# Performance work log

Hardware: AMD Instinct MI355X
Metric: run time of the kernel (lower is better)

The kernel has to match this reference:

```python
import jax, jax.numpy as jnp
import numpy as np

DIM = 1024
NUM_HEADS = 16
HEAD_DIM = DIM // NUM_HEADS
SCALE = HEAD_DIM ** -0.5
NEG = -1e9


def setup_inputs() -> dict:
    key = jax.random.key(0)
    ks = jax.random.split(key, 10)
    B, N, M, C = 8, 1024, 1024, DIM
    q = jax.random.normal(ks[0], (B, N, C), jnp.float32)
    k = jax.random.normal(ks[1], (B, M, C), jnp.float32)
    v = jax.random.normal(ks[2], (B, M, C), jnp.float32)
    mask = jax.random.randint(ks[3], (B, N), 0, 2, jnp.int32)
    target_mask = jax.random.randint(ks[4], (B, N, M), 0, 2, jnp.int32)
    Wq = jax.random.normal(ks[5], (C, C), jnp.float32) * 0.02
    Wk = jax.random.normal(ks[6], (C, C), jnp.float32) * 0.02
    Wv = jax.random.normal(ks[7], (C, C), jnp.float32) * 0.02
    Wo = jax.random.normal(ks[8], (C, C), jnp.float32) * 0.02
    bo = jnp.zeros((C,), jnp.float32)
    return {"q": q, "k": k, "v": v, "mask": mask, "target_mask": target_mask,
            "Wq": Wq, "Wk": Wk, "Wv": Wv, "Wo": Wo, "bo": bo}


def reference(q, k, v, mask, target_mask, Wq, Wk, Wv, Wo, bo):
    B, N, C = q.shape
    M = k.shape[1]
    H, D = NUM_HEADS, HEAD_DIM
    qh = (q @ Wq).reshape(B, N, H, D)
    kh = (k @ Wk).reshape(B, M, H, D)
    vh = (v @ Wv).reshape(B, M, H, D)
    attn = jnp.einsum('bnhd,bmhd->bhnm', qh, kh) * SCALE  # (B,H,N,M)
    # self-attn key mask (B,N) -> broadcast over queries (requires N==M as in original)
    attn = jnp.where(mask[:, None, None, :] == 0, NEG, attn)
    # cross-attn mask (B,N,M) -> broadcast over heads
    attn = jnp.where(target_mask[:, None, :, :] == 0, NEG, attn)
    attn = jax.nn.softmax(attn, axis=-1)
    x = jnp.einsum('bhnm,bmhd->bnhd', attn, vh).reshape(B, N, C)
    return x @ Wo + bo
```

## Files before the change

kernel.cpp:

```cpp
#include <hip/hip_runtime.h>
#include <hip/hip_bf16.h>

#define DEV __device__ __forceinline__

typedef __attribute__((ext_vector_type(8))) short bf16x8;
typedef __attribute__((ext_vector_type(4))) float f32x4;
typedef unsigned int u32;
typedef unsigned long long u64;

#define VMCNT(n) asm volatile("s_waitcnt vmcnt(" #n ")" ::: "memory")

DEV short f2bf(float f) {
  union { float f; u32 u; } x; x.f = f;
  u32 r = x.u + 0x7fffu + ((x.u >> 16) & 1u);
  return (short)(r >> 16);
}

DEV void gload_lds16(const void* g, void* l) {
  __builtin_amdgcn_global_load_lds(
      (const __attribute__((address_space(1))) u32*)g,
      (__attribute__((address_space(3))) u32*)l, 16, 0, 0);
}

DEV bf16x8 frag(const short* L, int row, int col) {
  return *(const bf16x8*)&L[row * 64 + (col ^ ((row & 7) << 3))];
}

DEV void stageA256(const char* base, int ktb, char* lds, int w, int lane) {
  int r8 = lane >> 3;
  int csw = ((lane & 7) ^ r8) << 4;
#pragma unroll
  for (int l = 0; l < 4; ++l) {
    int c = l * 8 + w;
    gload_lds16(base + (size_t)(c * 8 + r8) * 2048 + ktb + csw, lds + c * 1024);
  }
}
DEV void stageB128(const char* base, int ktb, char* lds, int w, int lane) {
  int r8 = lane >> 3;
  int csw = ((lane & 7) ^ r8) << 4;
#pragma unroll
  for (int l = 0; l < 2; ++l) {
    int c = l * 8 + w;
    gload_lds16(base + (size_t)(c * 8 + r8) * 2048 + ktb + csw, lds + c * 1024);
  }
}

DEV void tile_compute(const short* Asb, const short* Bsb, f32x4 acc[8][2],
                      int wm, int wn, int lr, int lg) {
  bf16x8 bfrag[2][2];
#pragma unroll
  for (int ni = 0; ni < 2; ++ni)
#pragma unroll
    for (int ks = 0; ks < 2; ++ks)
      bfrag[ni][ks] = frag(Bsb, wn * 32 + ni * 16 + lr, ks * 32 + lg * 8);
#pragma unroll
  for (int pi = 0; pi < 4; ++pi) {
    bf16x8 af[2][2];
#pragma unroll
    for (int m2 = 0; m2 < 2; ++m2)
#pragma unroll
      for (int ks = 0; ks < 2; ++ks)
        af[m2][ks] = frag(Asb, wm * 128 + (pi * 2 + m2) * 16 + lr, ks * 32 + lg * 8);
    __builtin_amdgcn_s_setprio(1);
#pragma unroll
    for (int m2 = 0; m2 < 2; ++m2)
#pragma unroll
      for (int ni = 0; ni < 2; ++ni)
#pragma unroll
        for (int ks = 0; ks < 2; ++ks)
          acc[pi * 2 + m2][ni] = __builtin_amdgcn_mfma_f32_16x16x32_bf16(
              af[m2][ks], bfrag[ni][ks], acc[pi * 2 + m2][ni], 0, 0, 0);
    __builtin_amdgcn_s_setprio(0);
  }
}

#define ENTRY_SYNC()                          \
  __builtin_amdgcn_sched_barrier(0);          \
  __builtin_amdgcn_s_barrier();               \
  __builtin_amdgcn_sched_barrier(0)

__global__ __launch_bounds__(256) void prologue(
    const float* __restrict__ q, const float* __restrict__ k, const float* __restrict__ v,
    short* __restrict__ qb, short* __restrict__ kb, short* __restrict__ vb,
    const float* __restrict__ W0, const float* __restrict__ W1,
    const float* __restrict__ W2, const float* __restrict__ W3,
    short* __restrict__ WtAll,
    const int* __restrict__ mask, const int* __restrict__ tmask, u64* __restrict__ pk) {
  int bx = blockIdx.x;
  if (bx < 12288) {
    int z = bx >> 12, bi = bx & 4095;
    const float* src = z == 0 ? q : z == 1 ? k : v;
    short* dst = z == 0 ? qb : z == 1 ? kb : vb;
    size_t i = ((size_t)bi * 256 + threadIdx.x) * 8;
    float4 f0 = *(const float4*)(src + i);
    float4 f1 = *(const float4*)(src + i + 4);
    bf16x8 o;
    o[0] = f2bf(f0.x); o[1] = f2bf(f0.y); o[2] = f2bf(f0.z); o[3] = f2bf(f0.w);
    o[4] = f2bf(f1.x); o[5] = f2bf(f1.y); o[6] = f2bf(f1.z); o[7] = f2bf(f1.w);
    *(bf16x8*)(dst + i) = o;
  } else if (bx < 13312) {
    int idx = bx - 12288;
    int z = idx >> 8, rem = idx & 255;
    const float* W = z == 0 ? W0 : z == 1 ? W1 : z == 2 ? W2 : W3;
    short* Wt = WtAll + (size_t)z * 1024 * 1024;
    __shared__ short tile[64][65];
    int k0 = (rem >> 4) * 64, n0 = (rem & 15) * 64;
    int t = threadIdx.x;
    int r = t >> 2, c = (t & 3) * 16;
    const float* src = W + (size_t)(k0 + r) * 1024 + n0 + c;
#pragma unroll
    for (int i = 0; i < 16; i += 4) {
      float4 f = *(const float4*)(src + i);
      tile[r][c + i + 0] = f2bf(f.x);
      tile[r][c + i + 1] = f2bf(f.y);
      tile[r][c + i + 2] = f2bf(f.z);
      tile[r][c + i + 3] = f2bf(f.w);
    }
    __syncthreads();
    bf16x8 v0, v1;
#pragma unroll
    for (int i = 0; i < 8; ++i) v0[i] = tile[c + i][r];
#pragma unroll
    for (int i = 0; i < 8; ++i) v1[i] = tile[c + 8 + i][r];
    short* dst = Wt + (size_t)(n0 + r) * 1024 + k0 + c;
    *(bf16x8*)(dst) = v0;
    *(bf16x8*)(dst + 8) = v1;
  } else {
    int bn = bx - 13312;
    int b = bn >> 10;
    int t = threadIdx.x, w = t >> 6, lane = t & 63;
    const int* tr = tmask + (size_t)bn * 1024;
    const int* mr = mask + b * 1024;
#pragma unroll
    for (int it = 0; it < 4; ++it) {
      int m = it * 256 + w * 64 + lane;
      bool on = (mr[m] != 0) && (tr[m] != 0);
      u64 bits = __ballot(on);
      if (lane == 0) pk[(size_t)bn * 16 + it * 4 + w] = bits;
    }
  }
}

__global__ __launch_bounds__(256) void vtrans(const short* __restrict__ vh,
                                              short* __restrict__ vht) {
  __shared__ short tile[64][65];
  int m0 = blockIdx.x * 64;
  int bh = blockIdx.y;
  int t = threadIdx.x;
  int r = t >> 2, c = (t & 3) * 16;
  const short* src = vh + ((size_t)bh * 1024 + m0 + r) * 64 + c;
  bf16x8 a0 = *(const bf16x8*)(src);
  bf16x8 a1 = *(const bf16x8*)(src + 8);
#pragma unroll
  for (int i = 0; i < 8; ++i) tile[r][c + i] = a0[i];
#pragma unroll
  for (int i = 0; i < 8; ++i) tile[r][c + 8 + i] = a1[i];
  __syncthreads();
  bf16x8 v0, v1;
#pragma unroll
  for (int i = 0; i < 8; ++i) v0[i] = tile[c + i][r];
#pragma unroll
  for (int i = 0; i < 8; ++i) v1[i] = tile[c + 8 + i][r];
  short* dst = vht + ((size_t)bh * 64 + r) * 1024 + m0 + c;
  *(bf16x8*)dst = v0;
  *(bf16x8*)(dst + 8) = v1;
}

#define QSCALE 0.18033688011112042f

__global__ __launch_bounds__(512, 2) void gemm_qkv(
    const short* __restrict__ qb, const short* __restrict__ kb, const short* __restrict__ vb,
    const short* __restrict__ WtAll,
    short* __restrict__ qh, short* __restrict__ kh, short* __restrict__ vh) {
  __shared__ __align__(16) short AsAll[3 * 256 * 64];
  __shared__ __align__(16) short BsAll[3 * 128 * 64];

  int flat = blockIdx.y * 8 + blockIdx.x;
  int nid = (flat & 7) * 96 + (flat >> 3);
  int zz = nid >> 8;
  int rr = nid & 255;
  int bm = (rr >> 3) * 256, bn = (rr & 7) * 128;

  const short* A; short* Ch; float cs;
  if (zz == 0)      { A = qb; Ch = qh; cs = QSCALE; }
  else if (zz == 1) { A = kb; Ch = kh; cs = 1.0f; }
  else              { A = vb; Ch = vh; cs = 1.0f; }
  const short* Wt = WtAll + (size_t)zz * 1024 * 1024;

  int tid = threadIdx.x;
  int lane = tid & 63, w = tid >> 6;
  int wm = w >> 2, wn = w & 3;
  int lr = lane & 15, lg = lane >> 4;

  const f32x4 fz = {0.f, 0.f, 0.f, 0.f};
  f32x4 acc[8][2];
#pragma unroll
  for (int i = 0; i < 8; ++i) { acc[i][0] = fz; acc[i][1] = fz; }

  const char* abase = (const char*)A + (size_t)bm * 2048;
  const char* bbase = (const char*)Wt + (size_t)bn * 2048;

  stageA256(abase, 0, (char*)AsAll, w, lane);
  stageB128(bbase, 0, (char*)BsAll, w, lane);
  stageA256(abase, 128, (char*)AsAll + 32768, w, lane);
  stageB128(bbase, 128, (char*)BsAll + 16384, w, lane);

  int cb = 0, sb = 2;
  for (int t = 0; t < 15; ++t) {
    VMCNT(6);
    ENTRY_SYNC();
    if (t < 14) {
      stageA256(abase, (t + 2) * 128, (char*)AsAll + sb * 32768, w, lane);
      stageB128(bbase, (t + 2) * 128, (char*)BsAll + sb * 16384, w, lane);
    }
    tile_compute(AsAll + cb * 16384, BsAll + cb * 8192, acc, wm, wn, lr, lg);
    cb = (cb == 2) ? 0 : cb + 1;
    sb = (sb == 2) ? 0 : sb + 1;
  }
  VMCNT(0);
  ENTRY_SYNC();
  tile_compute(AsAll + cb * 16384, BsAll + cb * 8192, acc, wm, wn, lr, lg);

#pragma unroll
  for (int mi = 0; mi < 8; ++mi)
#pragma unroll
    for (int ni = 0; ni < 2; ++ni) {
      int ccol = bn + wn * 32 + ni * 16 + lr;
      int h = ccol >> 6, d = ccol & 63;
#pragma unroll
      for (int j = 0; j < 4; ++j) {
        int r = bm + wm * 128 + mi * 16 + lg * 4 + j;
        int bb = r >> 10, n = r & 1023;
        Ch[(((size_t)bb * 16 + h) * 1024 + n) * 64 + d] = f2bf(acc[mi][ni][j] * cs);
      }
    }
}

__global__ __launch_bounds__(512, 2) void gemm_out(
    const short* __restrict__ X, const short* __restrict__ Wot,
    const float* __restrict__ bo, float* __restrict__ out) {
  __shared__ __align__(16) short AsAll[3 * 256 * 64];
  __shared__ __align__(16) short BsAll[3 * 128 * 64];

  int flat = blockIdx.y * 8 + blockIdx.x;
  int nid = (flat & 7) * 32 + (flat >> 3);
  int bm = (nid >> 3) * 256, bn = (nid & 7) * 128;

  int tid = threadIdx.x;
  int lane = tid & 63, w = tid >> 6;
  int wm = w >> 2, wn = w & 3;
  int lr = lane & 15, lg = lane >> 4;

  const f32x4 fz = {0.f, 0.f, 0.f, 0.f};
  f32x4 acc[8][2];
#pragma unroll
  for (int i = 0; i < 8; ++i) { acc[i][0] = fz; acc[i][1] = fz; }

  const char* abase = (const char*)X + (size_t)bm * 2048;
  const char* bbase = (const char*)Wot + (size_t)bn * 2048;

  stageA256(abase, 0, (char*)AsAll, w, lane);
  stageB128(bbase, 0, (char*)BsAll, w, lane);
  stageA256(abase, 128, (char*)AsAll + 32768, w, lane);
  stageB128(bbase, 128, (char*)BsAll + 16384, w, lane);

  int cb = 0, sb = 2;
  for (int t = 0; t < 15; ++t) {
    VMCNT(6);
    ENTRY_SYNC();
    if (t < 14) {
      stageA256(abase, (t + 2) * 128, (char*)AsAll + sb * 32768, w, lane);
      stageB128(bbase, (t + 2) * 128, (char*)BsAll + sb * 16384, w, lane);
    }
    tile_compute(AsAll + cb * 16384, BsAll + cb * 8192, acc, wm, wn, lr, lg);
    cb = (cb == 2) ? 0 : cb + 1;
    sb = (sb == 2) ? 0 : sb + 1;
  }
  VMCNT(0);
  ENTRY_SYNC();
  tile_compute(AsAll + cb * 16384, BsAll + cb * 8192, acc, wm, wn, lr, lg);

#pragma unroll
  for (int mi = 0; mi < 8; ++mi)
#pragma unroll
    for (int ni = 0; ni < 2; ++ni) {
      int ccol = bn + wn * 32 + ni * 16 + lr;
      float bias = bo[ccol];
#pragma unroll
      for (int j = 0; j < 4; ++j) {
        int r = bm + wm * 128 + mi * 16 + lg * 4 + j;
        out[(size_t)r * 1024 + ccol] = acc[mi][ni][j] + bias;
      }
    }
}

DEV void stage_kv(const char* kbase, const char* vbase, int kv0,
                  short* Ksb, short* Vsb, int w, int lane) {
#pragma unroll
  for (int i = 0; i < 2; ++i) {
    int c = w * 2 + i;
    int row = (lane >> 3);
    int colb = ((lane & 7) ^ row) << 4;
    gload_lds16(kbase + (size_t)(kv0 + c * 8 + row) * 128 + colb, (char*)Ksb + c * 1024);
    gload_lds16(vbase + (size_t)(c * 8 + row) * 2048 + kv0 * 2 + colb, (char*)Vsb + c * 1024);
  }
}

__global__ __launch_bounds__(256, 2) void attn(
    const short* __restrict__ qh, const short* __restrict__ kh, const short* __restrict__ vht,
    const u64* __restrict__ pk, short* __restrict__ x) {
  __shared__ __align__(16) short Ks[2][4096];
  __shared__ __align__(16) short Vs[2][4096];
  __shared__ __align__(16) short Ps[2][8192];

  int flat = blockIdx.y * 8 + blockIdx.x;
  int nid = (flat & 7) * 64 + (flat >> 3);
  int bh = nid >> 2, qp = nid & 3;
  int b = bh >> 4;
  int tid = threadIdx.x, lane = tid & 63, w = tid >> 6;
  int lr = lane & 15, lg = lane >> 4;

  bf16x8 qa[2][2][2];
#pragma unroll
  for (int sub = 0; sub < 2; ++sub) {
    const short* qb2 = qh + ((size_t)bh * 1024 + qp * 256 + sub * 128 + w * 32) * 64;
#pragma unroll
    for (int mi = 0; mi < 2; ++mi)
#pragma unroll
      for (int ks = 0; ks < 2; ++ks)
        qa[sub][mi][ks] = *(const bf16x8*)(qb2 + (mi * 16 + lr) * 64 + ks * 32 + lg * 8);
  }

  const f32x4 fz = {0.f, 0.f, 0.f, 0.f};
  f32x4 o[2][2][4];
  float psum[2][2][4];
#pragma unroll
  for (int sub = 0; sub < 2; ++sub)
#pragma unroll
    for (int mi = 0; mi < 2; ++mi)
#pragma unroll
      for (int j = 0; j < 4; ++j) { psum[sub][mi][j] = 0.f; o[sub][mi][j] = fz; }

  const char* kbase = (const char*)(kh + (size_t)bh * 65536);
  const char* vbase = (const char*)(vht + (size_t)bh * 65536);
  const u64* pkb = pk + ((size_t)b * 1024 + qp * 256) * 16;

  stage_kv(kbase, vbase, 0, Ks[0], Vs[0], w, lane);
  __syncthreads();
  int cur = 0;

  for (int t = 0; t < 16; ++t) {
    if (t < 15) stage_kv(kbase, vbase, (t + 1) * 64, Ks[cur ^ 1], Vs[cur ^ 1], w, lane);

#pragma unroll
    for (int sub = 0; sub < 2; ++sub) {
      u64 pw[2][4];
#pragma unroll
      for (int mi = 0; mi < 2; ++mi)
#pragma unroll
        for (int j = 0; j < 4; ++j)
          pw[mi][j] = pkb[(sub * 128 + w * 32 + mi * 16 + lg * 4 + j) * 16 + t];

      f32x4 s[2][4];
#pragma unroll
      for (int mi = 0; mi < 2; ++mi)
#pragma unroll
        for (int ni = 0; ni < 4; ++ni) s[mi][ni] = fz;
      __builtin_amdgcn_s_setprio(1);
#pragma unroll
      for (int ks = 0; ks < 2; ++ks) {
        bf16x8 kb2[4];
#pragma unroll
        for (int ni = 0; ni < 4; ++ni)
          kb2[ni] = *(const bf16x8*)&Ks[cur][(ni * 16 + lr) * 64 + ((ks * 32 + lg * 8) ^ ((lr & 7) << 3))];
#pragma unroll
        for (int mi = 0; mi < 2; ++mi)
#pragma unroll
          for (int ni = 0; ni < 4; ++ni)
            s[mi][ni] = __builtin_amdgcn_mfma_f32_16x16x32_bf16(qa[sub][mi][ks], kb2[ni], s[mi][ni], 0, 0, 0);
      }
      __builtin_amdgcn_s_setprio(0);

#pragma unroll
      for (int mi = 0; mi < 2; ++mi)
#pragma unroll
        for (int j = 0; j < 4; ++j) {
          u32 lo = (u32)pw[mi][j], hi = (u32)(pw[mi][j] >> 32);
          int r = w * 32 + mi * 16 + lg * 4 + j;
          int sw = (r & 7) << 3;
          float rs = 0.f;
#pragma unroll
          for (int ni = 0; ni < 4; ++ni) {
            u32 bit = ((ni < 2 ? lo : hi) >> ((ni & 1) * 16 + lr)) & 1u;
            float e = __builtin_amdgcn_exp2f(s[mi][ni][j]);
            float p = bit ? e : 0.f;
            rs += p;
            union { float f; u32 u; } cv; cv.f = p;
            Ps[sub][r * 64 + ((ni * 16 + lr) ^ sw)] = (short)((cv.u + 0x8000u) >> 16);
          }
          psum[sub][mi][j] += rs;
        }

      __builtin_amdgcn_s_setprio(1);
#pragma unroll
      for (int ks = 0; ks < 2; ++ks) {
        bf16x8 pa[2], vb2[4];
#pragma unroll
        for (int mi = 0; mi < 2; ++mi)
          pa[mi] = *(const bf16x8*)&Ps[sub][(w * 32 + mi * 16 + lr) * 64 + ((ks * 32 + lg * 8) ^ ((lr & 7) << 3))];
#pragma unroll
        for (int nd = 0; nd < 4; ++nd)
          vb2[nd] = *(const bf16x8*)&Vs[cur][(nd * 16 + lr) * 64 + ((ks * 32 + lg * 8) ^ ((lr & 7) << 3))];
#pragma unroll
        for (int mi = 0; mi < 2; ++mi)
#pragma unroll
          for (int nd = 0; nd < 4; ++nd)
            o[sub][mi][nd] = __builtin_amdgcn_mfma_f32_16x16x32_bf16(pa[mi], vb2[nd], o[sub][mi][nd], 0, 0, 0);
      }
      __builtin_amdgcn_s_setprio(0);
    }
    __syncthreads();
    cur ^= 1;
  }

  short* xb = x + ((size_t)b * 1024) * 1024 + (bh & 15) * 64;
#pragma unroll
  for (int sub = 0; sub < 2; ++sub)
#pragma unroll
    for (int mi = 0; mi < 2; ++mi)
#pragma unroll
      for (int j = 0; j < 4; ++j) {
        float rs = psum[sub][mi][j];
#pragma unroll
        for (int dd = 1; dd < 16; dd <<= 1) rs += __shfl_xor(rs, dd, 64);
        float inv = rs > 0.f ? 1.0f / rs : 0.f;
        int qg = qp * 256 + sub * 128 + w * 32 + mi * 16 + lg * 4 + j;
#pragma unroll
        for (int nd = 0; nd < 4; ++nd) {
          int d = nd * 16 + lr;
          xb[(size_t)qg * 1024 + d] = f2bf(o[sub][mi][nd][j] * inv);
        }
      }
}

extern "C" void kernel_launch(void* const* d_in, const int* in_sizes, int n_in,
                              void* d_out, int out_size, void* d_ws, size_t ws_size,
                              hipStream_t stream) {
  const float* q = (const float*)d_in[0];
  const float* k = (const float*)d_in[1];
  const float* v = (const float*)d_in[2];
  const int* mask = (const int*)d_in[3];
  const int* tmask = (const int*)d_in[4];
  const float* Wq = (const float*)d_in[5];
  const float* Wk = (const float*)d_in[6];
  const float* Wv = (const float*)d_in[7];
  const float* Wo = (const float*)d_in[8];
  const float* bo = (const float*)d_in[9];
  float* out = (float*)d_out;

  char* ws = (char*)d_ws;
  const size_t MB = 1u << 20;
  if (ws_size < 73 * MB) return;
  short* WtAll = (short*)(ws + 0 * MB);
  short* qh  = (short*)(ws + 8 * MB);
  short* kh  = (short*)(ws + 24 * MB);
  short* vh  = (short*)(ws + 40 * MB);
  short* vht = (short*)(ws + 56 * MB);
  u64*   pkb = (u64*)(ws + 72 * MB);
  short* x   = (short*)(ws + 40 * MB);
  short* qbA = (short*)d_out;
  short* kbA = (short*)d_out + 8 * 1024 * 1024;
  short* vbA = (short*)(ws + 56 * MB);

  prologue<<<dim3(21504), 256, 0, stream>>>(q, k, v, qbA, kbA, vbA,
                                            Wq, Wk, Wv, Wo, WtAll,
                                            mask, tmask, pkb);
  gemm_qkv<<<dim3(8, 96), 512, 0, stream>>>(qbA, kbA, vbA, WtAll, qh, kh, vh);
  vtrans<<<dim3(16, 128), 256, 0, stream>>>(vh, vht);
  attn<<<dim3(8, 64), 256, 0, stream>>>(qh, kh, vht, pkb, x);
  gemm_out<<<dim3(8, 32), 512, 0, stream>>>(x, WtAll + 3 * 1024 * 1024, bo, out);
}
```

Before: 356.4 us.

## Interleave global-to-LDS staging with MFMA phases in projection GEMM k-loop

Restructures the shared GEMM main loop used by the QKV projection and output projection kernels into four phases per k-tile. Each phase issues part of the next tile's global-to-LDS loads (A in halves, then B) between the fragment reads and the MFMAs, with barriers and lgkmcnt waits around each phase. The goal is to spread memory issue across the compute and keep waves in lockstep so load latency hides behind MFMA work. In exchange it adds two workgroup barriers per phase, eight per k-tile, which may cost more in synchronisation than the overlap recovers.

```diff
diff --git a/kernel.cpp b/kernel.cpp
--- a/kernel.cpp
+++ b/kernel.cpp
@@ -9,6 +9,13 @@
 typedef unsigned long long u64;
 
 #define VMCNT(n) asm volatile("s_waitcnt vmcnt(" #n ")" ::: "memory")
+#define LGK0()                                               \
+  asm volatile("s_waitcnt lgkmcnt(0)" ::: "memory");         \
+  __builtin_amdgcn_sched_barrier(0)
+#define ENTRY_SYNC()                          \
+  __builtin_amdgcn_sched_barrier(0);          \
+  __builtin_amdgcn_s_barrier();               \
+  __builtin_amdgcn_sched_barrier(0)
 
 DEV short f2bf(float f) {
   union { float f; u32 u; } x; x.f = f;
@@ -26,12 +33,12 @@
   return *(const bf16x8*)&L[row * 64 + (col ^ ((row & 7) << 3))];
 }
 
-DEV void stageA256(const char* base, int ktb, char* lds, int w, int lane) {
+DEV void stageA_half(const char* base, int ktb, char* lds, int w, int lane, int half) {
   int r8 = lane >> 3;
   int csw = ((lane & 7) ^ r8) << 4;
 #pragma unroll
-  for (int l = 0; l < 4; ++l) {
-    int c = l * 8 + w;
+  for (int l = 0; l < 2; ++l) {
+    int c = (half * 2 + l) * 8 + w;
     gload_lds16(base + (size_t)(c * 8 + r8) * 2048 + ktb + csw, lds + c * 1024);
   }
 }
@@ -45,39 +52,67 @@
   }
 }
 
-DEV void tile_compute(const short* Asb, const short* Bsb, f32x4 acc[8][2],
-                      int wm, int wn, int lr, int lg) {
-  bf16x8 bfrag[2][2];
-#pragma unroll
-  for (int ni = 0; ni < 2; ++ni)
-#pragma unroll
-    for (int ks = 0; ks < 2; ++ks)
-      bfrag[ni][ks] = frag(Bsb, wn * 32 + ni * 16 + lr, ks * 32 + lg * 8);
-#pragma unroll
-  for (int pi = 0; pi < 4; ++pi) {
-    bf16x8 af[2][2];
-#pragma unroll
-    for (int m2 = 0; m2 < 2; ++m2)
-#pragma unroll
-      for (int ks = 0; ks < 2; ++ks)
-        af[m2][ks] = frag(Asb, wm * 128 + (pi * 2 + m2) * 16 + lr, ks * 32 + lg * 8);
-    __builtin_amdgcn_s_setprio(1);
-#pragma unroll
-    for (int m2 = 0; m2 < 2; ++m2)
-#pragma unroll
-      for (int ni = 0; ni < 2; ++ni)
+DEV void kloop(const char* abase, const char* bbase, short* AsAll, short* BsAll,
+               f32x4 acc[8][2], int wm, int wn, int lr, int lg, int w, int lane) {
+  stageA_half(abase, 0, (char*)AsAll, w, lane, 0);
+  stageA_half(abase, 0, (char*)AsAll, w, lane, 1);
+  stageB128(bbase, 0, (char*)BsAll, w, lane);
+  stageA_half(abase, 128, (char*)AsAll + 32768, w, lane, 0);
+  stageA_half(abase, 128, (char*)AsAll + 32768, w, lane, 1);
+  stageB128(bbase, 128, (char*)BsAll + 16384, w, lane);
+  VMCNT(6);
+  ENTRY_SYNC();
+
+  int cb = 0, sb = 2;
+  for (int t = 0; t < 16; ++t) {
+    const short* Asb = AsAll + cb * 16384;
+    const short* Bsb = BsAll + cb * 8192;
+    char* sa = (char*)AsAll + sb * 32768;
+    char* sbb = (char*)BsAll + sb * 16384;
+    int ktb = (t + 2) * 128;
+    bf16x8 bfr[2][2];
+#pragma unroll
+    for (int p = 0; p < 4; ++p) {
+      if (p == 0) {
+#pragma unroll
+        for (int ni = 0; ni < 2; ++ni)
+#pragma unroll
+          for (int ks = 0; ks < 2; ++ks)
+            bfr[ni][ks] = frag(Bsb, wn * 32 + ni * 16 + lr, ks * 32 + lg * 8);
+      }
+      bf16x8 af[2][2];
+#pragma unroll
+      for (int m2 = 0; m2 < 2; ++m2)
 #pragma unroll
         for (int ks = 0; ks < 2; ++ks)
-          acc[pi * 2 + m2][ni] = __builtin_amdgcn_mfma_f32_16x16x32_bf16(
-              af[m2][ks], bfrag[ni][ks], acc[pi * 2 + m2][ni], 0, 0, 0);
-    __builtin_amdgcn_s_setprio(0);
-  }
-}
-
-#define ENTRY_SYNC()                          \
-  __builtin_amdgcn_sched_barrier(0);          \
-  __builtin_amdgcn_s_barrier();               \
-  __builtin_amdgcn_sched_barrier(0)
+          af[m2][ks] = frag(Asb, wm * 128 + (p * 2 + m2) * 16 + lr, ks * 32 + lg * 8);
+      if (t < 14) {
+        if (p == 0) stageA_half(abase, ktb, sa, w, lane, 0);
+        else if (p == 1) stageA_half(abase, ktb, sa, w, lane, 1);
+        else if (p == 2) stageB128(bbase, ktb, sbb, w, lane);
+      }
+      if (p == 3) {
+        if (t < 14) { VMCNT(6); }
+        else if (t == 14) { VMCNT(0); }
+      }
+      ENTRY_SYNC();
+      LGK0();
+      __builtin_amdgcn_s_setprio(1);
+#pragma unroll
+      for (int m2 = 0; m2 < 2; ++m2)
+#pragma unroll
+        for (int ni = 0; ni < 2; ++ni)
+#pragma unroll
+          for (int ks = 0; ks < 2; ++ks)
+            acc[p * 2 + m2][ni] = __builtin_amdgcn_mfma_f32_16x16x32_bf16(
+                af[m2][ks], bfr[ni][ks], acc[p * 2 + m2][ni], 0, 0, 0);
+      __builtin_amdgcn_s_setprio(0);
+      ENTRY_SYNC();
+    }
+    cb = (cb == 2) ? 0 : cb + 1;
+    sb = (sb == 2) ? 0 : sb + 1;
+  }
+}
 
 __global__ __launch_bounds__(256) void prologue(
     const float* __restrict__ q, const float* __restrict__ k, const float* __restrict__ v,
@@ -197,29 +232,8 @@
 #pragma unroll
   for (int i = 0; i < 8; ++i) { acc[i][0] = fz; acc[i][1] = fz; }
 
-  const char* abase = (const char*)A + (size_t)bm * 2048;
-  const char* bbase = (const char*)Wt + (size_t)bn * 2048;
-
-  stageA256(abase, 0, (char*)AsAll, w, lane);
-  stageB128(bbase, 0, (char*)BsAll, w, lane);
-  stageA256(abase, 128, (char*)AsAll + 32768, w, lane);
-  stageB128(bbase, 128, (char*)BsAll + 16384, w, lane);
-
-  int cb = 0, sb = 2;
-  for (int t = 0; t < 15; ++t) {
-    VMCNT(6);
-    ENTRY_SYNC();
-    if (t < 14) {
-      stageA256(abase, (t + 2) * 128, (char*)AsAll + sb * 32768, w, lane);
-      stageB128(bbase, (t + 2) * 128, (char*)BsAll + sb * 16384, w, lane);
-    }
-    tile_compute(AsAll + cb * 16384, BsAll + cb * 8192, acc, wm, wn, lr, lg);
-    cb = (cb == 2) ? 0 : cb + 1;
-    sb = (sb == 2) ? 0 : sb + 1;
-  }
-  VMCNT(0);
-  ENTRY_SYNC();
-  tile_compute(AsAll + cb * 16384, BsAll + cb * 8192, acc, wm, wn, lr, lg);
+  kloop((const char*)A + (size_t)bm * 2048, (const char*)Wt + (size_t)bn * 2048,
+        AsAll, BsAll, acc, wm, wn, lr, lg, w, lane);
 
 #pragma unroll
   for (int mi = 0; mi < 8; ++mi)
@@ -256,29 +270,8 @@
 #pragma unroll
   for (int i = 0; i < 8; ++i) { acc[i][0] = fz; acc[i][1] = fz; }
 
-  const char* abase = (const char*)X + (size_t)bm * 2048;
-  const char* bbase = (const char*)Wot + (size_t)bn * 2048;
-
-  stageA256(abase, 0, (char*)AsAll, w, lane);
-  stageB128(bbase, 0, (char*)BsAll, w, lane);
-  stageA256(abase, 128, (char*)AsAll + 32768, w, lane);
-  stageB128(bbase, 128, (char*)BsAll + 16384, w, lane);
-
-  int cb = 0, sb = 2;
-  for (int t = 0; t < 15; ++t) {
-    VMCNT(6);
-    ENTRY_SYNC();
-    if (t < 14) {
-      stageA256(abase, (t + 2) * 128, (char*)AsAll + sb * 32768, w, lane);
-      stageB128(bbase, (t + 2) * 128, (char*)BsAll + sb * 16384, w, lane);
-    }
-    tile_compute(AsAll + cb * 16384, BsAll + cb * 8192, acc, wm, wn, lr, lg);
-    cb = (cb == 2) ? 0 : cb + 1;
-    sb = (sb == 2) ? 0 : sb + 1;
-  }
-  VMCNT(0);
-  ENTRY_SYNC();
-  tile_compute(AsAll + cb * 16384, BsAll + cb * 8192, acc, wm, wn, lr, lg);
+  kloop((const char*)X + (size_t)bm * 2048, (const char*)Wot + (size_t)bn * 2048,
+        AsAll, BsAll, acc, wm, wn, lr, lg, w, lane);
 
 #pragma unroll
   for (int mi = 0; mi < 8; ++mi)
```

Result: no change. 360.1 us (+1.0%).
